# Optimization experiments

Hardware: AMD Instinct MI355X
Metric: run time of the kernel (lower is better)

Reference implementation:

```python
import jax, jax.numpy as jnp
import numpy as np

B, NOBJ = 64, 16
NUM_CLASSES = 91
IOU_TH = 0.5
NEG_POS = 3
VAR0, VAR1 = 0.1, 0.2
IMG = 300.0


def _ssd300_priors():
    # Standard SSD300 PriorBox: 8732 priors in center-size form (cx, cy, w, h), normalized to [0,1]
    fmaps = [38, 19, 10, 5, 3, 1]
    steps = [8, 16, 32, 64, 100, 300]
    min_s = [30, 60, 111, 162, 213, 264]
    max_s = [60, 111, 162, 213, 264, 315]
    ars = [[2], [2, 3], [2, 3], [2, 3], [2], [2]]
    out = []
    for k, f in enumerate(fmaps):
        for i in range(f):
            for j in range(f):
                cx = (j + 0.5) * steps[k] / IMG
                cy = (i + 0.5) * steps[k] / IMG
                s = min_s[k] / IMG
                out.append([cx, cy, s, s])
                sp = float(np.sqrt(s * max_s[k] / IMG))
                out.append([cx, cy, sp, sp])
                for ar in ars[k]:
                    r = float(np.sqrt(ar))
                    out.append([cx, cy, s * r, s / r])
                    out.append([cx, cy, s / r, s * r])
    return np.clip(np.asarray(out, np.float32), 0.0, 1.0)


def setup_inputs() -> dict:
    priors = jnp.asarray(_ssd300_priors())  # [8732, 4]
    P = priors.shape[0]
    key = jax.random.key(0)
    k1, k2, k3, k4, k5 = jax.random.split(key, 5)
    loc_data = jax.random.normal(k1, (B, P, 4), jnp.float32)
    conf_data = jax.random.normal(k2, (B, P, NUM_CLASSES), jnp.float32)
    centers = jax.random.uniform(k3, (B, NOBJ, 2), minval=40.0, maxval=260.0)
    half = jax.random.uniform(k5, (B, NOBJ, 2), minval=10.0, maxval=40.0)
    gt_boxes = jnp.concatenate([centers - half, centers + half], axis=-1)  # point form, pixel coords
    gt_labels = jax.random.randint(k4, (B, NOBJ), 1, NUM_CLASSES).astype(jnp.int32)
    return {"loc_data": loc_data, "conf_data": conf_data, "gt_boxes": gt_boxes,
            "gt_labels": gt_labels, "priors": priors}


def _point_form(pr):
    return jnp.concatenate([pr[:, :2] - pr[:, 2:] / 2, pr[:, :2] + pr[:, 2:] / 2], axis=1)


def _jaccard(boxes, pboxes):
    # boxes [N,4], pboxes [P,4] both point form -> IoU [N,P]
    lt = jnp.maximum(boxes[:, None, :2], pboxes[None, :, :2])
    rb = jnp.minimum(boxes[:, None, 2:], pboxes[None, :, 2:])
    wh = jnp.clip(rb - lt, 0.0)
    inter = wh[..., 0] * wh[..., 1]
    area_a = ((boxes[:, 2] - boxes[:, 0]) * (boxes[:, 3] - boxes[:, 1]))[:, None]
    area_b = ((pboxes[:, 2] - pboxes[:, 0]) * (pboxes[:, 3] - pboxes[:, 1]))[None, :]
    return inter / (area_a + area_b - inter)


def _encode(matched, priors):
    # matched [P,4] point form, priors [P,4] center-size form
    g_cxcy = ((matched[:, :2] + matched[:, 2:]) / 2 - priors[:, :2]) / (VAR0 * priors[:, 2:])
    g_wh = jnp.log((matched[:, 2:] - matched[:, :2]) / priors[:, 2:]) / VAR1
    return jnp.concatenate([g_cxcy, g_wh], axis=1)


def _match(boxes, labels, priors):
    # boxes [NOBJ,4] normalized point form; labels [NOBJ]; priors [P,4]
    ov = _jaccard(boxes, _point_form(priors))            # [NOBJ, P]
    best_prior_idx = jnp.argmax(ov, axis=1)              # [NOBJ]
    best_truth_ov = jnp.max(ov, axis=0)                  # [P]
    best_truth_idx = jnp.argmax(ov, axis=0)              # [P]
    best_truth_ov = best_truth_ov.at[best_prior_idx].set(2.0)
    for j in range(NOBJ):  # small fixed loop, matches torch in-order scatter
        best_truth_idx = best_truth_idx.at[best_prior_idx[j]].set(j)
    matched = boxes[best_truth_idx]                      # [P,4]
    conf = labels[best_truth_idx]
    conf = jnp.where(best_truth_ov < IOU_TH, 0, conf)
    return _encode(matched, priors), conf


def reference(loc_data, conf_data, gt_boxes, gt_labels, priors):
    P = priors.shape[0]
    loc_t, conf_t = jax.vmap(lambda b, l: _match(b / IMG, l, priors))(gt_boxes, gt_labels)
    pos = conf_t > 0                                      # [B,P]
    # localization loss: SmoothL1 (beta=1), summed over positives
    diff = loc_data - loc_t
    ad = jnp.abs(diff)
    sl1 = jnp.where(ad < 1.0, 0.5 * diff * diff, ad - 0.5)
    loss_l = jnp.sum(sl1 * pos[..., None].astype(sl1.dtype))
    # hard negative mining on per-prior CE loss
    lse = jax.nn.logsumexp(conf_data, axis=-1)            # [B,P]
    gathered = jnp.take_along_axis(conf_data, conf_t[..., None].astype(jnp.int32), axis=-1)[..., 0]
    ce_all = lse - gathered                                # [B,P]
    mine = jnp.where(pos, 0.0, ce_all)
    order = jnp.argsort(-mine, axis=1)
    rank = jnp.argsort(order, axis=1)
    num_pos = jnp.sum(pos, axis=1, keepdims=True)
    num_neg = jnp.clip(NEG_POS * num_pos, 1, P - 1)
    neg = rank < num_neg
    mask = pos | neg
    loss_c = jnp.sum(ce_all * mask.astype(ce_all.dtype))
    N = jnp.maximum(jnp.sum(num_pos).astype(jnp.float32), 1.0)
    return jnp.stack([loss_l / N, loss_c / N])  # [loss_l, loss_c]
```

## Files before the change

### kernel.cpp

```cpp
#include <hip/hip_runtime.h>
#include <math.h>

#define BATCH 64
#define NOBJ 16
#define NPRIOR 8732
#define NC 91
#define IMG 300.0f
#define GPB 1092
#define NGROUP (GPB * BATCH)
#define CE_GRID 6144
#define GBINS 2048
#define HB 16
#define HCHUNK 546
#define MSPLIT 16
#define SL 546

__global__ __launch_bounds__(256) void k_match_a(
    const float* __restrict__ gt_boxes,
    const float* __restrict__ priors,
    float* __restrict__ ov_g,
    unsigned char* __restrict__ idx_g,
    float* __restrict__ candv,
    int*   __restrict__ candi)
{
    __shared__ float bx0[NOBJ], by0[NOBJ], bx1[NOBJ], by1[NOBJ], barea[NOBJ];
    __shared__ float rv[NOBJ][4];
    __shared__ int   ri[NOBJ][4];

    const int b    = blockIdx.y;
    const int blk  = blockIdx.x;
    const int tid  = threadIdx.x;
    const int lane = tid & 63;
    const int wave = tid >> 6;
    const int p0   = blk * SL;
    const int pend = min(p0 + SL, NPRIOR);

    if (tid < NOBJ) {
        float4 g = ((const float4*)gt_boxes)[(size_t)b * NOBJ + tid];
        float x0 = g.x * (1.0f / IMG), y0 = g.y * (1.0f / IMG);
        float x1 = g.z * (1.0f / IMG), y1 = g.w * (1.0f / IMG);
        bx0[tid] = x0; by0[tid] = y0; bx1[tid] = x1; by1[tid] = y1;
        barea[tid] = (x1 - x0) * (y1 - y0);
    }
    __syncthreads();

    float bv[NOBJ];
    int   bi[NOBJ];
#pragma unroll
    for (int j = 0; j < NOBJ; j++) { bv[j] = -1.0f; bi[j] = 0x7fffffff; }

    for (int p = p0 + tid; p < pend; p += 256) {
        float4 pr = ((const float4*)priors)[p];
        float cx = pr.x, cy = pr.y, w = pr.z, h = pr.w;
        float px0 = cx - 0.5f * w, py0 = cy - 0.5f * h;
        float px1 = cx + 0.5f * w, py1 = cy + 0.5f * h;
        float pa = w * h;
        float maxv = -1.0f; int maxj = 0;
#pragma unroll
        for (int j = 0; j < NOBJ; j++) {
            float ltx = fmaxf(bx0[j], px0), lty = fmaxf(by0[j], py0);
            float rbx = fminf(bx1[j], px1), rby = fminf(by1[j], py1);
            float iw = fmaxf(rbx - ltx, 0.0f), ih = fmaxf(rby - lty, 0.0f);
            float inter = iw * ih;
            float iou = inter / (barea[j] + pa - inter);
            if (iou > maxv) { maxv = iou; maxj = j; }
            if (iou > bv[j]) { bv[j] = iou; bi[j] = p; }
        }
        ov_g[(size_t)b * NPRIOR + p]  = maxv;
        idx_g[(size_t)b * NPRIOR + p] = (unsigned char)maxj;
    }

#pragma unroll
    for (int j = 0; j < NOBJ; j++) {
        float v = bv[j]; int ix = bi[j];
        for (int off = 32; off; off >>= 1) {
            float v2 = __shfl_xor(v, off);
            int   i2 = __shfl_xor(ix, off);
            if (v2 > v || (v2 == v && i2 < ix)) { v = v2; ix = i2; }
        }
        if (lane == 0) { rv[j][wave] = v; ri[j][wave] = ix; }
    }
    __syncthreads();
    if (tid < NOBJ) {
        int j = tid;
        float v = rv[j][0]; int ix = ri[j][0];
#pragma unroll
        for (int w2 = 1; w2 < 4; w2++) {
            float v2 = rv[j][w2]; int i2 = ri[j][w2];
            if (v2 > v || (v2 == v && i2 < ix)) { v = v2; ix = i2; }
        }
        size_t o = ((size_t)b * MSPLIT + blk) * NOBJ + j;
        candv[o] = v;
        candi[o] = ix;
    }
}

__global__ __launch_bounds__(64) void k_bpi(
    const float* __restrict__ candv,
    const int*   __restrict__ candi,
    int* __restrict__ bpi_g)
{
    const int b = blockIdx.x;
    const int j = threadIdx.x;
    if (j < NOBJ) {
        size_t base = (size_t)b * MSPLIT * NOBJ + j;
        float v = candv[base]; int ix = candi[base];
#pragma unroll
        for (int c = 1; c < MSPLIT; c++) {
            float v2 = candv[base + c * NOBJ];
            int   i2 = candi[base + c * NOBJ];
            if (v2 > v || (v2 == v && i2 < ix)) { v = v2; ix = i2; }
        }
        bpi_g[b * NOBJ + j] = ix;
    }
}

__global__ __launch_bounds__(256) void k_match_c(
    const float* __restrict__ loc_data,
    const float* __restrict__ gt_boxes,
    const int*   __restrict__ gt_labels,
    const float* __restrict__ priors,
    const float* __restrict__ ov_g,
    const unsigned char* __restrict__ idx_g,
    const int*   __restrict__ bpi_g,
    int*   __restrict__ conf_t,
    float* __restrict__ ll_part,
    int*   __restrict__ np_part)
{
    __shared__ float bx0[NOBJ], by0[NOBJ], bx1[NOBJ], by1[NOBJ];
    __shared__ int   blab[NOBJ], bpi_s[NOBJ];
    __shared__ float red_f[4];
    __shared__ int   red_i[4];

    const int b    = blockIdx.y;
    const int blk  = blockIdx.x;
    const int tid  = threadIdx.x;
    const int lane = tid & 63;
    const int wave = tid >> 6;
    const int p0   = blk * SL;
    const int pend = min(p0 + SL, NPRIOR);

    if (tid < NOBJ) {
        float4 g = ((const float4*)gt_boxes)[(size_t)b * NOBJ + tid];
        bx0[tid] = g.x * (1.0f / IMG); by0[tid] = g.y * (1.0f / IMG);
        bx1[tid] = g.z * (1.0f / IMG); by1[tid] = g.w * (1.0f / IMG);
        blab[tid]  = gt_labels[b * NOBJ + tid];
        bpi_s[tid] = bpi_g[b * NOBJ + tid];
    }
    __syncthreads();

    int np_local = 0;
    float ll_local = 0.0f;
    for (int p = p0 + tid; p < pend; p += 256) {
        float ov = ov_g[(size_t)b * NPRIOR + p];
        int ti = (int)idx_g[(size_t)b * NPRIOR + p];
        int oj = -1;
#pragma unroll
        for (int j = 0; j < NOBJ; j++)
            if (bpi_s[j] == p) oj = j;
        int conf;
        if (oj >= 0) { ti = oj; conf = blab[oj]; }
        else         { conf = (ov < 0.5f) ? 0 : blab[ti]; }
        conf_t[(size_t)b * NPRIOR + p] = conf;
        if (conf > 0) {
            np_local++;
            float4 pr = ((const float4*)priors)[p];
            float cx = pr.x, cy = pr.y, w = pr.z, h = pr.w;
            float mx0 = bx0[ti], my0 = by0[ti], mx1 = bx1[ti], my1 = by1[ti];
            float g0 = ((mx0 + mx1) * 0.5f - cx) / (0.1f * w);
            float g1 = ((my0 + my1) * 0.5f - cy) / (0.1f * h);
            float g2 = logf((mx1 - mx0) / w) * 5.0f;
            float g3 = logf((my1 - my0) / h) * 5.0f;
            float4 lv = ((const float4*)loc_data)[(size_t)b * NPRIOR + p];
            float d0 = lv.x - g0, d1 = lv.y - g1, d2 = lv.z - g2, d3 = lv.w - g3;
            float a0 = fabsf(d0), a1 = fabsf(d1), a2 = fabsf(d2), a3 = fabsf(d3);
            ll_local += (a0 < 1.f ? 0.5f * d0 * d0 : a0 - 0.5f)
                      + (a1 < 1.f ? 0.5f * d1 * d1 : a1 - 0.5f)
                      + (a2 < 1.f ? 0.5f * d2 * d2 : a2 - 0.5f)
                      + (a3 < 1.f ? 0.5f * d3 * d3 : a3 - 0.5f);
        }
    }
    for (int off = 32; off; off >>= 1) {
        ll_local += __shfl_xor(ll_local, off);
        np_local += __shfl_xor(np_local, off);
    }
    if (lane == 0) { red_f[wave] = ll_local; red_i[wave] = np_local; }
    __syncthreads();
    if (tid == 0) {
        float ll = red_f[0] + red_f[1] + red_f[2] + red_f[3];
        int   np = red_i[0] + red_i[1] + red_i[2] + red_i[3];
        ll_part[b * MSPLIT + blk] = ll;
        np_part[b * MSPLIT + blk] = np;
    }
}


#define CE_ISSUE(gg, R0, R1, R2, NF)                                           \
    {   int b_ = (gg) / GPB, ci_ = (gg) - b_ * GPB;                            \
        int p0_ = ci_ * 8;                                                     \
        int rows_ = min(8, NPRIOR - p0_);                                      \
        NF = (rows_ * NC) >> 2;                                                \
        const float4* s_ = (const float4*)(conf_data + ((size_t)b_ * NPRIOR + p0_) * NC); \
        R0 = s_[tid];                                                          \
        if (tid + 64  < NF) R1 = s_[tid + 64];                                 \
        if (tid + 128 < NF) R2 = s_[tid + 128]; }

#define CT_LOAD(gg)                                                            \
    ( conf_t[(size_t)((gg) / GPB) * NPRIOR + ((gg) - ((gg) / GPB) * GPB) * 8 + (tid >> 3)] )

#define CE_WRITE(BUF, R0, R1, R2, NF)                                          \
    {   float4* d_ = (float4*)sbuf[BUF];                                       \
        d_[tid] = R0;                                                          \
        if (tid + 64  < NF) d_[tid + 64]  = R1;                                \
        if (tid + 128 < NF) d_[tid + 128] = R2; }

#define CE_COMPUTE(gg, BUF, TG)                                                \
    {   int b_ = (gg) / GPB, ci_ = (gg) - b_ * GPB;                            \
        int p0_ = ci_ * 8;                                                     \
        int rows_ = min(8, NPRIOR - p0_);                                      \
        int rr_ = tid >> 3, q_ = tid & 7;                                      \
        if (rr_ < rows_) {                                                     \
            const float* row_ = sbuf[BUF] + rr_ * NC;                          \
            float s_ = 0.0f;                                                   \
            _Pragma("unroll")                                                  \
            for (int i_ = q_; i_ < NC; i_ += 8) s_ += __expf(row_[i_]);        \
            s_ += __shfl_xor(s_, 1);                                           \
            s_ += __shfl_xor(s_, 2);                                           \
            s_ += __shfl_xor(s_, 4);                                           \
            if (q_ == 0) {                                                     \
                size_t o_ = (size_t)b_ * NPRIOR + p0_ + rr_;                   \
                int tgt_ = TG;                                                 \
                float ce_ = __logf(s_) - row_[tgt_];                           \
                if (tgt_ > 0) { pos_acc += ce_; mine[o_] = 0.0f; }             \
                else          { mine[o_] = fmaxf(ce_, 0.0f); }                 \
            } } }

__global__ __launch_bounds__(64) void k_ce(
    const float* __restrict__ conf_data,
    const int*   __restrict__ conf_t,
    float* __restrict__ mine,
    float* __restrict__ lc_part)
{
    __shared__ float sbuf[2][8 * NC];
    const int tid = threadIdx.x;
    const int G = CE_GRID;

    float4 a0, a1, a2, b0, b1, b2;
    int nfA = 0, nfB = 0;
    float pos_acc = 0.0f;

    int g = blockIdx.x;
    CE_ISSUE(g, a0, a1, a2, nfA);
    int tcur = CT_LOAD(g);
    if (g + G < NGROUP) CE_ISSUE(g + G, b0, b1, b2, nfB);
    CE_WRITE(0, a0, a1, a2, nfA);

    for (; g < NGROUP; g += 2 * G) {
        int tnext = (g + G < NGROUP) ? CT_LOAD(g + G) : 0;
        if (g + 2 * G < NGROUP) CE_ISSUE(g + 2 * G, a0, a1, a2, nfA);
        CE_COMPUTE(g, 0, tcur);
        if (g + G < NGROUP) {
            CE_WRITE(1, b0, b1, b2, nfB);
            int tn2 = (g + 2 * G < NGROUP) ? CT_LOAD(g + 2 * G) : 0;
            if (g + 3 * G < NGROUP) CE_ISSUE(g + 3 * G, b0, b1, b2, nfB);
            CE_COMPUTE(g + G, 1, tnext);
            if (g + 2 * G < NGROUP) CE_WRITE(0, a0, a1, a2, nfA);
            tcur = tn2;
        }
    }

    for (int off = 32; off; off >>= 1) pos_acc += __shfl_xor(pos_acc, off);
    if (tid == 0) lc_part[blockIdx.x] = pos_acc;
}

__global__ __launch_bounds__(256) void k_hist(
    const float* __restrict__ mine,
    int*   __restrict__ ghc,
    float* __restrict__ gsc)
{
    __shared__ int   lh[GBINS];
    __shared__ float ls[GBINS];

    const int b  = blockIdx.y;
    const int ci = blockIdx.x;
    const int tid = threadIdx.x;
    const int i0 = ci * HCHUNK;
    const int iend = min(i0 + HCHUNK, NPRIOR);

#pragma unroll
    for (int j = 0; j < GBINS / 256; j++) {
        lh[tid + j * 256] = 0;
        ls[tid + j * 256] = 0.0f;
    }
    __syncthreads();

    for (int i = i0 + tid; i < iend; i += 256) {
        float v = mine[(size_t)b * NPRIOR + i];
        int bin = min((int)(v * 128.0f), GBINS - 1);
        atomicAdd(&lh[bin], 1);
        atomicAdd(&ls[bin], v);
    }
    __syncthreads();

    const size_t base = ((size_t)b * HB + ci) * GBINS;
#pragma unroll
    for (int j = 0; j < GBINS / 256; j++) {
        int bin = tid + j * 256;
        ghc[base + bin] = lh[bin];
        gsc[base + bin] = ls[bin];
    }
}

__global__ __launch_bounds__(1024) void k_sel(
    const int*   __restrict__ ghc,
    const float* __restrict__ gsc,
    const int*   __restrict__ np_part,
    float* __restrict__ lc2)
{
    __shared__ int   wtot[16];
    __shared__ int   s_B0, s_r;
    __shared__ float red_f[16];

    const int b = blockIdx.x;
    const int tid = threadIdx.x;
    const int lane = tid & 63;
    const int wave = tid >> 6;

    int   c0 = 0, c1 = 0;
    float m0 = 0.0f, m1 = 0.0f;
    const size_t base = (size_t)b * HB * GBINS;
#pragma unroll
    for (int c = 0; c < HB; c++) {
        c0 += ghc[base + (size_t)c * GBINS + 2 * tid];
        c1 += ghc[base + (size_t)c * GBINS + 2 * tid + 1];
        m0 += gsc[base + (size_t)c * GBINS + 2 * tid];
        m1 += gsc[base + (size_t)c * GBINS + 2 * tid + 1];
    }

    int np = 0;
#pragma unroll
    for (int c = 0; c < MSPLIT; c++) np += np_part[b * MSPLIT + c];
    const int kk = min(max(3 * np, 1), NPRIOR - 1);

    const int ps = c0 + c1;
    int incl = ps;
#pragma unroll
    for (int off = 1; off < 64; off <<= 1) {
        int t = __shfl_down(incl, off);
        incl += (lane + off < 64) ? t : 0;
    }
    if (lane == 0) wtot[wave] = incl;
    __syncthreads();
    int hi = 0;
#pragma unroll
    for (int w = 0; w < 16; w++) if (w > wave) hi += wtot[w];
    const int suf = (incl - ps) + hi;
    if (suf < kk && kk <= suf + c1)          { s_B0 = 2 * tid + 1; s_r = kk - suf; }
    const int suf1 = suf + c1;
    if (suf1 < kk && kk <= suf1 + c0)        { s_B0 = 2 * tid;     s_r = kk - suf1; }
    __syncthreads();

    const int B0 = s_B0;
    const int r  = s_r;

    float sg = 0.0f;
    if (2 * tid     > B0) sg += m0;
    if (2 * tid + 1 > B0) sg += m1;
    if      (2 * tid     == B0) sg += (float)r * (m0 / (float)c0);
    else if (2 * tid + 1 == B0) sg += (float)r * (m1 / (float)c1);

    for (int off = 32; off; off >>= 1) sg += __shfl_xor(sg, off);
    if (lane == 0) red_f[wave] = sg;
    __syncthreads();
    if (tid == 0) {
        float s = 0.0f;
#pragma unroll
        for (int w = 0; w < 16; w++) s += red_f[w];
        lc2[b] = s;
    }
}

__global__ __launch_bounds__(1024) void k_final(
    const float* __restrict__ lc_part, const float* __restrict__ lc2,
    const float* __restrict__ ll_part, const int* __restrict__ np_part,
    float* __restrict__ out)
{
    __shared__ float rf[16][2];
    __shared__ int   rn[16];
    const int tid = threadIdx.x;
    float lc = 0.0f;
    for (int i = tid; i < CE_GRID; i += 1024) lc += lc_part[i];
    float ll = 0.0f; int np = 0;
    if (tid < BATCH) lc += lc2[tid];
    if (tid < BATCH * MSPLIT) { ll = ll_part[tid]; np = np_part[tid]; }
    for (int off = 32; off; off >>= 1) {
        lc += __shfl_xor(lc, off);
        ll += __shfl_xor(ll, off);
        np += __shfl_xor(np, off);
    }
    const int lane = tid & 63, wave = tid >> 6;
    if (lane == 0) { rf[wave][0] = lc; rf[wave][1] = ll; rn[wave] = np; }
    __syncthreads();
    if (tid == 0) {
        float lcT = 0.0f, llT = 0.0f; int npT = 0;
        for (int w = 0; w < 16; w++) { lcT += rf[w][0]; llT += rf[w][1]; npT += rn[w]; }
        float N = fmaxf((float)npT, 1.0f);
        out[0] = llT / N;
        out[1] = lcT / N;
    }
}

extern "C" void kernel_launch(void* const* d_in, const int* in_sizes, int n_in,
                              void* d_out, int out_size, void* d_ws, size_t ws_size,
                              hipStream_t stream)
{
    const float* loc_data  = (const float*)d_in[0];
    const float* conf_data = (const float*)d_in[1];
    const float* gt_boxes  = (const float*)d_in[2];
    const int*   gt_labels = (const int*)d_in[3];
    const float* priors    = (const float*)d_in[4];
    float* out = (float*)d_out;

    char* ws = (char*)d_ws;
    float* ll_part  = (float*)(ws + 0);
    int*   np_part  = (int*)(ws + 4096);
    float* lc2      = (float*)(ws + 8192);
    float* lc_part  = (float*)(ws + 12288);
    int*   conf_t   = (int*)(ws + 65536);
    float* mine     = (float*)(ws + 65536 + 2235392);
    float* ov_g     = (float*)(ws + 4536320);
    unsigned char* idx_g = (unsigned char*)(ws + 6771712);
    float* candv    = (float*)(ws + 7340032);
    int*   candi    = (int*)(ws + 7405568);
    int*   bpi_g    = (int*)(ws + 7471104);
    int*   ghc      = (int*)(ws + 16777216);
    float* gsc      = (float*)(ws + 25165824);

    hipLaunchKernelGGL(k_match_a, dim3(MSPLIT, BATCH), dim3(256), 0, stream,
                       gt_boxes, priors, ov_g, idx_g, candv, candi);
    hipLaunchKernelGGL(k_bpi, dim3(BATCH), dim3(64), 0, stream,
                       candv, candi, bpi_g);
    hipLaunchKernelGGL(k_match_c, dim3(MSPLIT, BATCH), dim3(256), 0, stream,
                       loc_data, gt_boxes, gt_labels, priors, ov_g, idx_g,
                       bpi_g, conf_t, ll_part, np_part);
    hipLaunchKernelGGL(k_ce, dim3(CE_GRID), dim3(64), 0, stream,
                       conf_data, conf_t, mine, lc_part);
    hipLaunchKernelGGL(k_hist, dim3(HB, BATCH), dim3(256), 0, stream,
                       mine, ghc, gsc);
    hipLaunchKernelGGL(k_sel, dim3(BATCH), dim3(1024), 0, stream,
                       ghc, gsc, np_part, lc2);
    hipLaunchKernelGGL(k_final, dim3(1), dim3(1024), 0, stream,
                       lc_part, lc2, ll_part, np_part, out);
}
```

Measured before the change: 100.6 us.

## Fuse matching passes and patch forced best-prior matches in a tiny fixup kernel

The IoU matching pass now computes conf_t and the localization loss directly from each prior's best ground-truth box, so the ov_g and idx_g intermediates and the second full matching pass are no longer needed. A small per-image fixup kernel then handles the forced best-prior-per-object matches. It overwrites conf_t at those priors and adds loss and positive-count deltas, which k_sel and k_final fold in. This removes a global round trip and a full-grid kernel, at the cost of a corrective step whose duplicate-index handling must reproduce the reference's last-writer semantics.

Measured after the change: 104.7 us. 1.04x slower.

```diff
diff --git a/kernel.cpp b/kernel.cpp
--- a/kernel.cpp
+++ b/kernel.cpp
@@ -15,17 +15,23 @@
 #define MSPLIT 16
 #define SL 546
 
-__global__ __launch_bounds__(256) void k_match_a(
+__global__ __launch_bounds__(256) void k_match1(
+    const float* __restrict__ loc_data,
     const float* __restrict__ gt_boxes,
+    const int*   __restrict__ gt_labels,
     const float* __restrict__ priors,
-    float* __restrict__ ov_g,
-    unsigned char* __restrict__ idx_g,
+    int*   __restrict__ conf_t,
+    float* __restrict__ ll_part,
+    int*   __restrict__ np_part,
     float* __restrict__ candv,
     int*   __restrict__ candi)
 {
     __shared__ float bx0[NOBJ], by0[NOBJ], bx1[NOBJ], by1[NOBJ], barea[NOBJ];
+    __shared__ int   blab[NOBJ];
     __shared__ float rv[NOBJ][4];
     __shared__ int   ri[NOBJ][4];
+    __shared__ float red_f[4];
+    __shared__ int   red_i[4];
 
     const int b    = blockIdx.y;
     const int blk  = blockIdx.x;
@@ -41,6 +47,7 @@
         float x1 = g.z * (1.0f / IMG), y1 = g.w * (1.0f / IMG);
         bx0[tid] = x0; by0[tid] = y0; bx1[tid] = x1; by1[tid] = y1;
         barea[tid] = (x1 - x0) * (y1 - y0);
+        blab[tid] = gt_labels[b * NOBJ + tid];
     }
     __syncthreads();
 
@@ -48,6 +55,9 @@
     int   bi[NOBJ];
 #pragma unroll
     for (int j = 0; j < NOBJ; j++) { bv[j] = -1.0f; bi[j] = 0x7fffffff; }
+
+    int np_local = 0;
+    float ll_local = 0.0f;
 
     for (int p = p0 + tid; p < pend; p += 256) {
         float4 pr = ((const float4*)priors)[p];
@@ -56,6 +66,7 @@
         float px1 = cx + 0.5f * w, py1 = cy + 0.5f * h;
         float pa = w * h;
         float maxv = -1.0f; int maxj = 0;
+        float mx0 = 0, my0 = 0, mx1 = 0, my1 = 0;
 #pragma unroll
         for (int j = 0; j < NOBJ; j++) {
             float ltx = fmaxf(bx0[j], px0), lty = fmaxf(by0[j], py0);
@@ -63,110 +74,16 @@
             float iw = fmaxf(rbx - ltx, 0.0f), ih = fmaxf(rby - lty, 0.0f);
             float inter = iw * ih;
             float iou = inter / (barea[j] + pa - inter);
-            if (iou > maxv) { maxv = iou; maxj = j; }
+            if (iou > maxv) {
+                maxv = iou; maxj = j;
+                mx0 = bx0[j]; my0 = by0[j]; mx1 = bx1[j]; my1 = by1[j];
+            }
             if (iou > bv[j]) { bv[j] = iou; bi[j] = p; }
         }
-        ov_g[(size_t)b * NPRIOR + p]  = maxv;
-        idx_g[(size_t)b * NPRIOR + p] = (unsigned char)maxj;
-    }
-
-#pragma unroll
-    for (int j = 0; j < NOBJ; j++) {
-        float v = bv[j]; int ix = bi[j];
-        for (int off = 32; off; off >>= 1) {
-            float v2 = __shfl_xor(v, off);
-            int   i2 = __shfl_xor(ix, off);
-            if (v2 > v || (v2 == v && i2 < ix)) { v = v2; ix = i2; }
-        }
-        if (lane == 0) { rv[j][wave] = v; ri[j][wave] = ix; }
-    }
-    __syncthreads();
-    if (tid < NOBJ) {
-        int j = tid;
-        float v = rv[j][0]; int ix = ri[j][0];
-#pragma unroll
-        for (int w2 = 1; w2 < 4; w2++) {
-            float v2 = rv[j][w2]; int i2 = ri[j][w2];
-            if (v2 > v || (v2 == v && i2 < ix)) { v = v2; ix = i2; }
-        }
-        size_t o = ((size_t)b * MSPLIT + blk) * NOBJ + j;
-        candv[o] = v;
-        candi[o] = ix;
-    }
-}
-
-__global__ __launch_bounds__(64) void k_bpi(
-    const float* __restrict__ candv,
-    const int*   __restrict__ candi,
-    int* __restrict__ bpi_g)
-{
-    const int b = blockIdx.x;
-    const int j = threadIdx.x;
-    if (j < NOBJ) {
-        size_t base = (size_t)b * MSPLIT * NOBJ + j;
-        float v = candv[base]; int ix = candi[base];
-#pragma unroll
-        for (int c = 1; c < MSPLIT; c++) {
-            float v2 = candv[base + c * NOBJ];
-            int   i2 = candi[base + c * NOBJ];
-            if (v2 > v || (v2 == v && i2 < ix)) { v = v2; ix = i2; }
-        }
-        bpi_g[b * NOBJ + j] = ix;
-    }
-}
-
-__global__ __launch_bounds__(256) void k_match_c(
-    const float* __restrict__ loc_data,
-    const float* __restrict__ gt_boxes,
-    const int*   __restrict__ gt_labels,
-    const float* __restrict__ priors,
-    const float* __restrict__ ov_g,
-    const unsigned char* __restrict__ idx_g,
-    const int*   __restrict__ bpi_g,
-    int*   __restrict__ conf_t,
-    float* __restrict__ ll_part,
-    int*   __restrict__ np_part)
-{
-    __shared__ float bx0[NOBJ], by0[NOBJ], bx1[NOBJ], by1[NOBJ];
-    __shared__ int   blab[NOBJ], bpi_s[NOBJ];
-    __shared__ float red_f[4];
-    __shared__ int   red_i[4];
-
-    const int b    = blockIdx.y;
-    const int blk  = blockIdx.x;
-    const int tid  = threadIdx.x;
-    const int lane = tid & 63;
-    const int wave = tid >> 6;
-    const int p0   = blk * SL;
-    const int pend = min(p0 + SL, NPRIOR);
-
-    if (tid < NOBJ) {
-        float4 g = ((const float4*)gt_boxes)[(size_t)b * NOBJ + tid];
-        bx0[tid] = g.x * (1.0f / IMG); by0[tid] = g.y * (1.0f / IMG);
-        bx1[tid] = g.z * (1.0f / IMG); by1[tid] = g.w * (1.0f / IMG);
-        blab[tid]  = gt_labels[b * NOBJ + tid];
-        bpi_s[tid] = bpi_g[b * NOBJ + tid];
-    }
-    __syncthreads();
-
-    int np_local = 0;
-    float ll_local = 0.0f;
-    for (int p = p0 + tid; p < pend; p += 256) {
-        float ov = ov_g[(size_t)b * NPRIOR + p];
-        int ti = (int)idx_g[(size_t)b * NPRIOR + p];
-        int oj = -1;
-#pragma unroll
-        for (int j = 0; j < NOBJ; j++)
-            if (bpi_s[j] == p) oj = j;
-        int conf;
-        if (oj >= 0) { ti = oj; conf = blab[oj]; }
-        else         { conf = (ov < 0.5f) ? 0 : blab[ti]; }
+        int conf = (maxv < 0.5f) ? 0 : blab[maxj];
         conf_t[(size_t)b * NPRIOR + p] = conf;
         if (conf > 0) {
             np_local++;
-            float4 pr = ((const float4*)priors)[p];
-            float cx = pr.x, cy = pr.y, w = pr.z, h = pr.w;
-            float mx0 = bx0[ti], my0 = by0[ti], mx1 = bx1[ti], my1 = by1[ti];
             float g0 = ((mx0 + mx1) * 0.5f - cx) / (0.1f * w);
             float g1 = ((my0 + my1) * 0.5f - cy) / (0.1f * h);
             float g2 = logf((mx1 - mx0) / w) * 5.0f;
@@ -180,20 +97,142 @@
                       + (a3 < 1.f ? 0.5f * d3 * d3 : a3 - 0.5f);
         }
     }
+
+#pragma unroll
+    for (int j = 0; j < NOBJ; j++) {
+        float v = bv[j]; int ix = bi[j];
+        for (int off = 32; off; off >>= 1) {
+            float v2 = __shfl_xor(v, off);
+            int   i2 = __shfl_xor(ix, off);
+            if (v2 > v || (v2 == v && i2 < ix)) { v = v2; ix = i2; }
+        }
+        if (lane == 0) { rv[j][wave] = v; ri[j][wave] = ix; }
+    }
     for (int off = 32; off; off >>= 1) {
         ll_local += __shfl_xor(ll_local, off);
         np_local += __shfl_xor(np_local, off);
     }
     if (lane == 0) { red_f[wave] = ll_local; red_i[wave] = np_local; }
     __syncthreads();
+    if (tid < NOBJ) {
+        int j = tid;
+        float v = rv[j][0]; int ix = ri[j][0];
+#pragma unroll
+        for (int w2 = 1; w2 < 4; w2++) {
+            float v2 = rv[j][w2]; int i2 = ri[j][w2];
+            if (v2 > v || (v2 == v && i2 < ix)) { v = v2; ix = i2; }
+        }
+        size_t o = ((size_t)b * MSPLIT + blk) * NOBJ + j;
+        candv[o] = v;
+        candi[o] = ix;
+    }
     if (tid == 0) {
-        float ll = red_f[0] + red_f[1] + red_f[2] + red_f[3];
-        int   np = red_i[0] + red_i[1] + red_i[2] + red_i[3];
-        ll_part[b * MSPLIT + blk] = ll;
-        np_part[b * MSPLIT + blk] = np;
-    }
-}
-
+        ll_part[b * MSPLIT + blk] = red_f[0] + red_f[1] + red_f[2] + red_f[3];
+        np_part[b * MSPLIT + blk] = red_i[0] + red_i[1] + red_i[2] + red_i[3];
+    }
+}
+
+__global__ __launch_bounds__(64) void k_bpi(
+    const float* __restrict__ candv,
+    const int*   __restrict__ candi,
+    int* __restrict__ bpi_g)
+{
+    const int b = blockIdx.x;
+    const int j = threadIdx.x;
+    if (j < NOBJ) {
+        size_t base = (size_t)b * MSPLIT * NOBJ + j;
+        float v = candv[base]; int ix = candi[base];
+#pragma unroll
+        for (int c = 1; c < MSPLIT; c++) {
+            float v2 = candv[base + c * NOBJ];
+            int   i2 = candi[base + c * NOBJ];
+            if (v2 > v || (v2 == v && i2 < ix)) { v = v2; ix = i2; }
+        }
+        bpi_g[b * NOBJ + j] = ix;
+    }
+}
+
+__global__ __launch_bounds__(64) void k_fix(
+    const float* __restrict__ loc_data,
+    const float* __restrict__ gt_boxes,
+    const int*   __restrict__ gt_labels,
+    const float* __restrict__ priors,
+    const int*   __restrict__ bpi_g,
+    int*   __restrict__ conf_t,
+    float* __restrict__ ll_fix,
+    int*   __restrict__ np_fix)
+{
+    const int b = blockIdx.x;
+    const int lane = threadIdx.x;
+
+    float ll_d = 0.0f;
+    int   np_d = 0;
+
+    if (lane < NOBJ) {
+        const int j = lane;
+        const int ps = bpi_g[b * NOBJ + j];
+        bool last = true;
+        for (int j2 = j + 1; j2 < NOBJ; j2++)
+            if (bpi_g[b * NOBJ + j2] == ps) last = false;
+        if (last) {
+            float4 pr = ((const float4*)priors)[ps];
+            float cx = pr.x, cy = pr.y, w = pr.z, h = pr.w;
+            float px0 = cx - 0.5f * w, py0 = cy - 0.5f * h;
+            float px1 = cx + 0.5f * w, py1 = cy + 0.5f * h;
+            float pa = w * h;
+            float maxv = -1.0f;
+            float mx0 = 0, my0 = 0, mx1 = 0, my1 = 0;
+            float jx0 = 0, jy0 = 0, jx1 = 0, jy1 = 0;
+            for (int j2 = 0; j2 < NOBJ; j2++) {
+                float4 g = ((const float4*)gt_boxes)[(size_t)b * NOBJ + j2];
+                float x0 = g.x * (1.0f / IMG), y0 = g.y * (1.0f / IMG);
+                float x1 = g.z * (1.0f / IMG), y1 = g.w * (1.0f / IMG);
+                float area = (x1 - x0) * (y1 - y0);
+                float ltx = fmaxf(x0, px0), lty = fmaxf(y0, py0);
+                float rbx = fminf(x1, px1), rby = fminf(y1, py1);
+                float iw = fmaxf(rbx - ltx, 0.0f), ih = fmaxf(rby - lty, 0.0f);
+                float inter = iw * ih;
+                float iou = inter / (area + pa - inter);
+                if (iou > maxv) { maxv = iou; mx0 = x0; my0 = y0; mx1 = x1; my1 = y1; }
+                if (j2 == j)    { jx0 = x0; jy0 = y0; jx1 = x1; jy1 = y1; }
+            }
+            float4 lv = ((const float4*)loc_data)[(size_t)b * NPRIOR + ps];
+            if (maxv >= 0.5f) {
+                float g0 = ((mx0 + mx1) * 0.5f - cx) / (0.1f * w);
+                float g1 = ((my0 + my1) * 0.5f - cy) / (0.1f * h);
+                float g2 = logf((mx1 - mx0) / w) * 5.0f;
+                float g3 = logf((my1 - my0) / h) * 5.0f;
+                float d0 = lv.x - g0, d1 = lv.y - g1, d2 = lv.z - g2, d3 = lv.w - g3;
+                float a0 = fabsf(d0), a1 = fabsf(d1), a2 = fabsf(d2), a3 = fabsf(d3);
+                ll_d -= (a0 < 1.f ? 0.5f * d0 * d0 : a0 - 0.5f)
+                      + (a1 < 1.f ? 0.5f * d1 * d1 : a1 - 0.5f)
+                      + (a2 < 1.f ? 0.5f * d2 * d2 : a2 - 0.5f)
+                      + (a3 < 1.f ? 0.5f * d3 * d3 : a3 - 0.5f);
+                np_d -= 1;
+            }
+            {
+                float g0 = ((jx0 + jx1) * 0.5f - cx) / (0.1f * w);
+                float g1 = ((jy0 + jy1) * 0.5f - cy) / (0.1f * h);
+                float g2 = logf((jx1 - jx0) / w) * 5.0f;
+                float g3 = logf((jy1 - jy0) / h) * 5.0f;
+                float d0 = lv.x - g0, d1 = lv.y - g1, d2 = lv.z - g2, d3 = lv.w - g3;
+                float a0 = fabsf(d0), a1 = fabsf(d1), a2 = fabsf(d2), a3 = fabsf(d3);
+                ll_d += (a0 < 1.f ? 0.5f * d0 * d0 : a0 - 0.5f)
+                      + (a1 < 1.f ? 0.5f * d1 * d1 : a1 - 0.5f)
+                      + (a2 < 1.f ? 0.5f * d2 * d2 : a2 - 0.5f)
+                      + (a3 < 1.f ? 0.5f * d3 * d3 : a3 - 0.5f);
+                np_d += 1;
+            }
+            conf_t[(size_t)b * NPRIOR + ps] = gt_labels[b * NOBJ + j];
+        }
+    }
+
+    for (int off = 32; off; off >>= 1) {
+        ll_d += __shfl_xor(ll_d, off);
+        np_d += __shfl_xor(np_d, off);
+    }
+    if (lane == 0) { ll_fix[b] = ll_d; np_fix[b] = np_d; }
+}
 
 #define CE_ISSUE(gg, R0, R1, R2, NF)                                           \
     {   int b_ = (gg) / GPB, ci_ = (gg) - b_ * GPB;                            \
@@ -315,6 +354,7 @@
     const int*   __restrict__ ghc,
     const float* __restrict__ gsc,
     const int*   __restrict__ np_part,
+    const int*   __restrict__ np_fix,
     float* __restrict__ lc2)
 {
     __shared__ int   wtot[16];
@@ -337,7 +377,7 @@
         m1 += gsc[base + (size_t)c * GBINS + 2 * tid + 1];
     }
 
-    int np = 0;
+    int np = np_fix[b];
 #pragma unroll
     for (int c = 0; c < MSPLIT; c++) np += np_part[b * MSPLIT + c];
     const int kk = min(max(3 * np, 1), NPRIOR - 1);
@@ -383,6 +423,7 @@
 __global__ __launch_bounds__(1024) void k_final(
     const float* __restrict__ lc_part, const float* __restrict__ lc2,
     const float* __restrict__ ll_part, const int* __restrict__ np_part,
+    const float* __restrict__ ll_fix, const int* __restrict__ np_fix,
     float* __restrict__ out)
 {
     __shared__ float rf[16][2];
@@ -391,8 +432,8 @@
     float lc = 0.0f;
     for (int i = tid; i < CE_GRID; i += 1024) lc += lc_part[i];
     float ll = 0.0f; int np = 0;
-    if (tid < BATCH) lc += lc2[tid];
-    if (tid < BATCH * MSPLIT) { ll = ll_part[tid]; np = np_part[tid]; }
+    if (tid < BATCH) { lc += lc2[tid]; ll += ll_fix[tid]; np += np_fix[tid]; }
+    if (tid < BATCH * MSPLIT) { ll += ll_part[tid]; np += np_part[tid]; }
     for (int off = 32; off; off >>= 1) {
         lc += __shfl_xor(lc, off);
         ll += __shfl_xor(ll, off);
@@ -425,30 +466,31 @@
     float* ll_part  = (float*)(ws + 0);
     int*   np_part  = (int*)(ws + 4096);
     float* lc2      = (float*)(ws + 8192);
+    float* ll_fix   = (float*)(ws + 8704);
+    int*   np_fix   = (int*)(ws + 9216);
     float* lc_part  = (float*)(ws + 12288);
     int*   conf_t   = (int*)(ws + 65536);
     float* mine     = (float*)(ws + 65536 + 2235392);
-    float* ov_g     = (float*)(ws + 4536320);
-    unsigned char* idx_g = (unsigned char*)(ws + 6771712);
     float* candv    = (float*)(ws + 7340032);
     int*   candi    = (int*)(ws + 7405568);
     int*   bpi_g    = (int*)(ws + 7471104);
     int*   ghc      = (int*)(ws + 16777216);
     float* gsc      = (float*)(ws + 25165824);
 
-    hipLaunchKernelGGL(k_match_a, dim3(MSPLIT, BATCH), dim3(256), 0, stream,
-                       gt_boxes, priors, ov_g, idx_g, candv, candi);
+    hipLaunchKernelGGL(k_match1, dim3(MSPLIT, BATCH), dim3(256), 0, stream,
+                       loc_data, gt_boxes, gt_labels, priors,
+                       conf_t, ll_part, np_part, candv, candi);
     hipLaunchKernelGGL(k_bpi, dim3(BATCH), dim3(64), 0, stream,
                        candv, candi, bpi_g);
-    hipLaunchKernelGGL(k_match_c, dim3(MSPLIT, BATCH), dim3(256), 0, stream,
-                       loc_data, gt_boxes, gt_labels, priors, ov_g, idx_g,
-                       bpi_g, conf_t, ll_part, np_part);
+    hipLaunchKernelGGL(k_fix, dim3(BATCH), dim3(64), 0, stream,
+                       loc_data, gt_boxes, gt_labels, priors, bpi_g,
+                       conf_t, ll_fix, np_fix);
     hipLaunchKernelGGL(k_ce, dim3(CE_GRID), dim3(64), 0, stream,
                        conf_data, conf_t, mine, lc_part);
     hipLaunchKernelGGL(k_hist, dim3(HB, BATCH), dim3(256), 0, stream,
                        mine, ghc, gsc);
     hipLaunchKernelGGL(k_sel, dim3(BATCH), dim3(1024), 0, stream,
-                       ghc, gsc, np_part, lc2);
+                       ghc, gsc, np_part, np_fix, lc2);
     hipLaunchKernelGGL(k_final, dim3(1), dim3(1024), 0, stream,
-                       lc_part, lc2, ll_part, np_part, out);
-}
+                       lc_part, lc2, ll_part, np_part, ll_fix, np_fix, out);
+}
```
